# Optimization experiments

Hardware: AMD Instinct MI355X
Metric: run time of the kernel (lower is better)

The kernel has to match this reference:

```python
import jax, jax.numpy as jnp
import numpy as np

D_MODEL = 1024
NUM_HEADS = 16
HEAD_DIM = D_MODEL // NUM_HEADS
BATCH, SEQ = 2, 2048


def setup_inputs() -> dict:
    key = jax.random.key(0)
    ks = jax.random.split(key, 11)
    s = 1.0 / np.sqrt(D_MODEL)
    inp = {
        "query": jax.random.normal(ks[0], (BATCH, SEQ, D_MODEL), jnp.float32),
        "key": jax.random.normal(ks[1], (BATCH, SEQ, D_MODEL), jnp.float32),
        "value": jax.random.normal(ks[2], (BATCH, SEQ, D_MODEL), jnp.float32),
        "q_w": jax.random.uniform(ks[3], (D_MODEL, D_MODEL), jnp.float32, -s, s),
        "q_b": jax.random.uniform(ks[4], (D_MODEL,), jnp.float32, -s, s),
        "k_w": jax.random.uniform(ks[5], (D_MODEL, D_MODEL), jnp.float32, -s, s),
        "k_b": jax.random.uniform(ks[6], (D_MODEL,), jnp.float32, -s, s),
        "v_w": jax.random.uniform(ks[7], (D_MODEL, D_MODEL), jnp.float32, -s, s),
        "v_b": jax.random.uniform(ks[8], (D_MODEL,), jnp.float32, -s, s),
        "o_w": jax.random.uniform(ks[9], (D_MODEL, D_MODEL), jnp.float32, -s, s),
        "o_b": jax.random.uniform(ks[10], (D_MODEL,), jnp.float32, -s, s),
    }
    return inp


def reference(query, key, value, q_w, q_b, k_w, k_b, v_w, v_b, o_w, o_b):
    B = query.shape[0]
    # linear projections (torch Linear: x @ W^T + b)
    q = query @ q_w.T + q_b
    k = key @ k_w.T + k_b
    v = value @ v_w.T + v_b
    # split heads: [B, S, D] -> [B, H, S, Hd]
    def split(x):
        return x.reshape(B, -1, NUM_HEADS, HEAD_DIM).transpose(0, 2, 1, 3)
    q, k, v = split(q), split(k), split(v)
    scores = jnp.einsum("bhqd,bhkd->bhqk", q, k) / np.sqrt(HEAD_DIM).astype(np.float32)
    attn = jax.nn.softmax(scores, axis=-1)
    out = jnp.einsum("bhqk,bhkd->bhqd", attn, v)  # [B,H,S,Hd]
    merged = out.transpose(0, 2, 1, 3).reshape(B, -1, D_MODEL)
    return merged @ o_w.T + o_b
```

## Files before the change

kernel.cpp:

```cpp
#include <hip/hip_runtime.h>
#include <hip/hip_bf16.h>

typedef unsigned short u16;
typedef unsigned int u32;
typedef __attribute__((ext_vector_type(8))) short short8;
typedef __attribute__((ext_vector_type(4))) short s16x4;
typedef __attribute__((ext_vector_type(4))) float f32x4;
typedef __attribute__((ext_vector_type(4))) u32 u32v4;

__device__ __forceinline__ u16 f2bf(float f) {
    u32 u = __float_as_uint(f);
    return (u16)((u + 0x7FFFu + ((u >> 16) & 1u)) >> 16);
}
__device__ __forceinline__ u32 pack2bf(float a, float b) {
    __hip_bfloat162 h = __float22bfloat162_rn(float2{a, b});
    return *reinterpret_cast<u32*>(&h);
}
__device__ __forceinline__ float exp2hw(float x) {
    float r;
    asm("v_exp_f32 %0, %1" : "=v"(r) : "v"(x));
    return r;
}

__device__ __forceinline__ void gload16(const void* g, void* s) {
    __builtin_amdgcn_global_load_lds(
        (const __attribute__((address_space(1))) void*)g,
        (__attribute__((address_space(3))) void*)s, 16, 0, 0);
}

__global__ __launch_bounds__(256) void cast_all_kernel(
    const float* __restrict__ s0, const float* __restrict__ s1, const float* __restrict__ s2,
    const float* __restrict__ s3, const float* __restrict__ s4, const float* __restrict__ s5,
    const float* __restrict__ s6,
    u16* __restrict__ d0, u16* __restrict__ d1, u16* __restrict__ d2,
    u16* __restrict__ d3, u16* __restrict__ d4, u16* __restrict__ d5,
    u16* __restrict__ d6, int nBig, int nSmall)
{
    const int y = blockIdx.y;
    const float* s = y == 0 ? s0 : (y == 1 ? s1 : (y == 2 ? s2 : (y == 3 ? s3 : (y == 4 ? s4 : (y == 5 ? s5 : s6)))));
    u16* d = y == 0 ? d0 : (y == 1 ? d1 : (y == 2 ? d2 : (y == 3 ? d3 : (y == 4 ? d4 : (y == 5 ? d5 : d6)))));
    const int n = (y < 3) ? nBig : nSmall;
    int i = (blockIdx.x * 256 + threadIdx.x) * 4;
    const int stride = gridDim.x * 256 * 4;
    for (; i < n; i += stride) {
        float4 v = *(const float4*)(s + i);
        uint2 t;
        t.x = pack2bf(v.x, v.y);
        t.y = pack2bf(v.z, v.w);
        *(uint2*)(d + i) = t;
    }
}

__global__ __launch_bounds__(256) void qkv_gemm(
    const u16* __restrict__ Xq, const u16* __restrict__ Xk, const u16* __restrict__ Xv,
    const u16* __restrict__ Wqkv,
    const float* __restrict__ qb, const float* __restrict__ kb, const float* __restrict__ vb,
    u16* __restrict__ Qo, u16* __restrict__ Ko, u16* __restrict__ Vo)
{
    constexpr int K = 1024;
    __shared__ __align__(16) u16 Asm[2][4096];
    __shared__ __align__(16) u16 Bsm[2][4096];

    const int tid = threadIdx.x;
    const int wid = tid >> 6;
    const int lane = tid & 63;
    const int r15 = lane & 15, g = lane >> 4;
    const int flat = blockIdx.x;
    const int z = flat >> 8;
    const int fb = flat & 255;
    const int lsw = (fb & 7) * 32 + (fb >> 3);
    const int m0 = (lsw >> 3) * 128, n0 = (lsw & 7) * 128;
    const int nAll = (z << 10) + n0;
    const u16* A = z == 0 ? Xq : (z == 1 ? Xk : Xv);
    const int wr = wid >> 1, wc = wid & 1;

    f32x4 acc[4][4];
#pragma unroll
    for (int i = 0; i < 4; ++i)
#pragma unroll
        for (int j = 0; j < 4; ++j) acc[i][j] = (f32x4){0.f, 0.f, 0.f, 0.f};

    const int idx0 = tid, idx1 = tid + 256;
    const size_t aoff0 = (size_t)(m0 + (idx0 >> 2)) * K + (idx0 & 3) * 8;
    const size_t aoff1 = (size_t)(m0 + (idx1 >> 2)) * K + (idx1 & 3) * 8;
    const size_t boff0 = (size_t)(nAll + (idx0 >> 2)) * K + (idx0 & 3) * 8;
    const size_t boff1 = (size_t)(nAll + (idx1 >> 2)) * K + (idx1 & 3) * 8;
    const u16* abase = &Asm[0][0] + (wr * 64 + r15) * 32 + g * 8;
    const u16* bbase = &Bsm[0][0] + (wc * 64 + r15) * 32 + g * 8;

    gload16(A + aoff0, &Asm[0][wid * 512]);
    gload16(A + aoff1, &Asm[0][2048 + wid * 512]);
    gload16(Wqkv + boff0, &Bsm[0][wid * 512]);
    gload16(Wqkv + boff1, &Bsm[0][2048 + wid * 512]);
    __syncthreads();

#pragma unroll 2
    for (int t = 0; t < 32; ++t) {
        const int buf = t & 1;
        if (t < 31) {
            const int kt = (t + 1) * 32;
            gload16(A + aoff0 + kt, &Asm[buf ^ 1][wid * 512]);
            gload16(A + aoff1 + kt, &Asm[buf ^ 1][2048 + wid * 512]);
            gload16(Wqkv + boff0 + kt, &Bsm[buf ^ 1][wid * 512]);
            gload16(Wqkv + boff1 + kt, &Bsm[buf ^ 1][2048 + wid * 512]);
        }
        short8 af[4], bfr[4];
#pragma unroll
        for (int i = 0; i < 4; ++i) {
            af[i]  = *(const short8*)(abase + buf * 4096 + i * 512);
            bfr[i] = *(const short8*)(bbase + buf * 4096 + i * 512);
        }
#pragma unroll
        for (int i = 0; i < 4; ++i)
#pragma unroll
            for (int j = 0; j < 4; ++j)
                acc[i][j] = __builtin_amdgcn_mfma_f32_16x16x32_bf16(af[i], bfr[j], acc[i][j], 0, 0, 0);
        __syncthreads();
    }

    const float scale = (z == 0) ? 0.125f * 1.4426950408889634f : 1.0f;
    u16* ob = z == 0 ? Qo : (z == 1 ? Ko : Vo);
    const float* bias = z == 0 ? qb : (z == 1 ? kb : vb);
#pragma unroll
    for (int i = 0; i < 4; ++i) {
        const int mbase = m0 + wr * 64 + i * 16 + g * 4;
#pragma unroll
        for (int j = 0; j < 4; ++j) {
            const int n = n0 + wc * 64 + j * 16 + r15;
            const float bb = bias[n];
            if (z < 2) {
#pragma unroll
                for (int r = 0; r < 4; ++r)
                    ob[(size_t)(mbase + r) * 1024 + n] = f2bf((acc[i][j][r] + bb) * scale);
            } else {
                const int b_ = mbase >> 11, s_ = mbase & 2047;
                const int blk = (s_ >> 2) & 7;
                const int pb = ((blk & 3) << 1) | (blk >> 2);
                const int s_new = (s_ & ~31) | (pb << 2);
                s16x4 pk;
#pragma unroll
                for (int r = 0; r < 4; ++r) pk[r] = (short)f2bf(acc[i][j][r] + bb);
                *(s16x4*)(ob + ((size_t)b_ << 21) + (size_t)n * 2048 + s_new) = pk;
            }
        }
    }
}

__global__ __launch_bounds__(256) void o_gemm(
    const u16* __restrict__ A, const u16* __restrict__ W,
    const float* __restrict__ bias, float* __restrict__ outp)
{
    constexpr int N = 1024, K = 1024;
    __shared__ __align__(16) u16 Asm[2][4096];
    __shared__ __align__(16) u16 Bsm[2][4096];
    const int tid = threadIdx.x;
    const int wid = tid >> 6;
    const int lane = tid & 63;
    const int r15 = lane & 15, g = lane >> 4;
    const int fb = blockIdx.y * 8 + blockIdx.x;
    const int lsw = (fb & 7) * 32 + (fb >> 3);
    const int m0 = (lsw >> 3) * 128, n0 = (lsw & 7) * 128;
    const int wr = wid >> 1, wc = wid & 1;

    f32x4 acc[4][4];
#pragma unroll
    for (int i = 0; i < 4; ++i)
#pragma unroll
        for (int j = 0; j < 4; ++j) acc[i][j] = (f32x4){0.f, 0.f, 0.f, 0.f};

    const int idx0 = tid, idx1 = tid + 256;
    const size_t aoff0 = (size_t)(m0 + (idx0 >> 2)) * K + (idx0 & 3) * 8;
    const size_t aoff1 = (size_t)(m0 + (idx1 >> 2)) * K + (idx1 & 3) * 8;
    const size_t boff0 = (size_t)(n0 + (idx0 >> 2)) * K + (idx0 & 3) * 8;
    const size_t boff1 = (size_t)(n0 + (idx1 >> 2)) * K + (idx1 & 3) * 8;
    const u16* abase = &Asm[0][0] + (wr * 64 + r15) * 32 + g * 8;
    const u16* bbase = &Bsm[0][0] + (wc * 64 + r15) * 32 + g * 8;

    gload16(A + aoff0, &Asm[0][wid * 512]);
    gload16(A + aoff1, &Asm[0][2048 + wid * 512]);
    gload16(W + boff0, &Bsm[0][wid * 512]);
    gload16(W + boff1, &Bsm[0][2048 + wid * 512]);
    __syncthreads();

#pragma unroll 2
    for (int t = 0; t < 32; ++t) {
        const int buf = t & 1;
        if (t < 31) {
            const int kt = (t + 1) * 32;
            gload16(A + aoff0 + kt, &Asm[buf ^ 1][wid * 512]);
            gload16(A + aoff1 + kt, &Asm[buf ^ 1][2048 + wid * 512]);
            gload16(W + boff0 + kt, &Bsm[buf ^ 1][wid * 512]);
            gload16(W + boff1 + kt, &Bsm[buf ^ 1][2048 + wid * 512]);
        }
        short8 af[4], bfr[4];
#pragma unroll
        for (int i = 0; i < 4; ++i) {
            af[i]  = *(const short8*)(abase + buf * 4096 + i * 512);
            bfr[i] = *(const short8*)(bbase + buf * 4096 + i * 512);
        }
#pragma unroll
        for (int i = 0; i < 4; ++i)
#pragma unroll
            for (int j = 0; j < 4; ++j)
                acc[i][j] = __builtin_amdgcn_mfma_f32_16x16x32_bf16(af[i], bfr[j], acc[i][j], 0, 0, 0);
        __syncthreads();
    }

#pragma unroll
    for (int i = 0; i < 4; ++i) {
        const int mbase = m0 + wr * 64 + i * 16 + g * 4;
#pragma unroll
        for (int j = 0; j < 4; ++j) {
            const int n = n0 + wc * 64 + j * 16 + r15;
            const float bb = bias[n];
#pragma unroll
            for (int r = 0; r < 4; ++r)
                outp[(size_t)(mbase + r) * N + n] = acc[i][j][r] + bb;
        }
    }
}

__global__ __launch_bounds__(256) void attn_kernel(
    const u16* __restrict__ Q, const u16* __restrict__ Kb,
    const u16* __restrict__ Vt, u16* __restrict__ Mo)
{
    __shared__ __align__(16) u16 Ksm[2][4096];
    __shared__ __align__(16) u16 Vsm[2][4096];
    const int tid = threadIdx.x;
    const int wid = tid >> 6, lane = tid & 63;
    const int r15 = lane & 15, g = lane >> 4;
    const int bid = blockIdx.x;
    const int l = (bid & 7) * 64 + (bid >> 3);
    const int bh = l >> 4;
    const int b = bh >> 4, h = bh & 15;
    const int q0 = (l & 15) * 128 + wid * 32;

    const u16* Qbase = Q + ((size_t)b * 2048 + q0) * 1024 + h * 64;
    short8 qf[2][2];
#pragma unroll
    for (int qt = 0; qt < 2; ++qt)
#pragma unroll
        for (int f = 0; f < 2; ++f)
            qf[qt][f] = *(const short8*)(Qbase + (size_t)(qt * 16 + r15) * 1024 + f * 32 + g * 8);

    const int p0 = tid, p1 = tid + 256;
    const int row0 = p0 >> 3, slot0s = (p0 & 7) ^ (row0 & 7);
    const int row1 = p1 >> 3, slot1s = (p1 & 7) ^ (row1 & 7);
    const u16* Ks0 = Kb + ((size_t)b * 2048 + row0) * 1024 + h * 64 + slot0s * 8;
    const u16* Ks1 = Kb + ((size_t)b * 2048 + row1) * 1024 + h * 64 + slot1s * 8;
    const u16* Vs0 = Vt + ((size_t)b << 21) + (size_t)(h * 64 + row0) * 2048 + slot0s * 8;
    const u16* Vs1 = Vt + ((size_t)b << 21) + (size_t)(h * 64 + row1) * 2048 + slot1s * 8;

    const int sA = r15 & 7;
    const int sl0 = (g ^ sA) * 8;
    const int sl1 = sl0 ^ 32;
    const u16* kb0 = &Ksm[0][0] + r15 * 64 + sl0;
    const u16* kb1 = &Ksm[0][0] + r15 * 64 + sl1;
    const u16* vb0 = &Vsm[0][0] + r15 * 64 + sl0;
    const u16* vb1 = &Vsm[0][0] + r15 * 64 + sl1;

    f32x4 acc[2][4];
#pragma unroll
    for (int qt = 0; qt < 2; ++qt)
#pragma unroll
        for (int d4 = 0; d4 < 4; ++d4) acc[qt][d4] = (f32x4){0.f, 0.f, 0.f, 0.f};
    f32x4 accl[2] = {(f32x4){0.f, 0.f, 0.f, 0.f}, (f32x4){0.f, 0.f, 0.f, 0.f}};
    const short8 vone = {0x3F80, 0x3F80, 0x3F80, 0x3F80, 0x3F80, 0x3F80, 0x3F80, 0x3F80};

    gload16(Ks0, &Ksm[0][wid * 512]);
    gload16(Ks1, &Ksm[0][2048 + wid * 512]);
    gload16(Vs0, &Vsm[0][wid * 512]);
    gload16(Vs1, &Vsm[0][2048 + wid * 512]);
    Ks0 += 65536; Ks1 += 65536; Vs0 += 64; Vs1 += 64;
    __syncthreads();

#pragma unroll 2
    for (int t = 0; t < 32; ++t) {
        const int buf = t & 1;
        if (t < 31) {
            gload16(Ks0, &Ksm[buf ^ 1][wid * 512]);
            gload16(Ks1, &Ksm[buf ^ 1][2048 + wid * 512]);
            gload16(Vs0, &Vsm[buf ^ 1][wid * 512]);
            gload16(Vs1, &Vsm[buf ^ 1][2048 + wid * 512]);
            Ks0 += 65536; Ks1 += 65536; Vs0 += 64; Vs1 += 64;
        }

        short8 kf[4][2];
#pragma unroll
        for (int kt = 0; kt < 4; ++kt) {
            kf[kt][0] = *(const short8*)(kb0 + buf * 4096 + kt * 1024);
            kf[kt][1] = *(const short8*)(kb1 + buf * 4096 + kt * 1024);
        }

        f32x4 st[2][4];
#pragma unroll
        for (int qt = 0; qt < 2; ++qt)
#pragma unroll
            for (int kt = 0; kt < 4; ++kt) {
                f32x4 zz = (f32x4){0.f, 0.f, 0.f, 0.f};
                zz = __builtin_amdgcn_mfma_f32_16x16x32_bf16(kf[kt][0], qf[qt][0], zz, 0, 0, 0);
                zz = __builtin_amdgcn_mfma_f32_16x16x32_bf16(kf[kt][1], qf[qt][1], zz, 0, 0, 0);
                st[qt][kt] = zz;
            }

        u32v4 pA[2], pB[2];
#pragma unroll
        for (int qt = 0; qt < 2; ++qt) {
#pragma unroll
            for (int kt = 0; kt < 4; ++kt) {
                float e0 = exp2hw(st[qt][kt][0]);
                float e1 = exp2hw(st[qt][kt][1]);
                float e2 = exp2hw(st[qt][kt][2]);
                float e3 = exp2hw(st[qt][kt][3]);
                u32 lo = pack2bf(e0, e1);
                u32 hi = pack2bf(e2, e3);
                if (kt < 2) { pA[qt][kt * 2] = lo; pA[qt][kt * 2 + 1] = hi; }
                else        { pB[qt][(kt - 2) * 2] = lo; pB[qt][(kt - 2) * 2 + 1] = hi; }
            }
        }

        accl[0] = __builtin_amdgcn_mfma_f32_16x16x32_bf16(vone, __builtin_bit_cast(short8, pA[0]), accl[0], 0, 0, 0);
        accl[0] = __builtin_amdgcn_mfma_f32_16x16x32_bf16(vone, __builtin_bit_cast(short8, pB[0]), accl[0], 0, 0, 0);
        accl[1] = __builtin_amdgcn_mfma_f32_16x16x32_bf16(vone, __builtin_bit_cast(short8, pA[1]), accl[1], 0, 0, 0);
        accl[1] = __builtin_amdgcn_mfma_f32_16x16x32_bf16(vone, __builtin_bit_cast(short8, pB[1]), accl[1], 0, 0, 0);

#pragma unroll
        for (int d4 = 0; d4 < 4; ++d4) {
            short8 vf0 = *(const short8*)(vb0 + buf * 4096 + d4 * 1024);
            short8 vf1 = *(const short8*)(vb1 + buf * 4096 + d4 * 1024);
            acc[0][d4] = __builtin_amdgcn_mfma_f32_16x16x32_bf16(vf0, __builtin_bit_cast(short8, pA[0]), acc[0][d4], 0, 0, 0);
            acc[0][d4] = __builtin_amdgcn_mfma_f32_16x16x32_bf16(vf1, __builtin_bit_cast(short8, pB[0]), acc[0][d4], 0, 0, 0);
            acc[1][d4] = __builtin_amdgcn_mfma_f32_16x16x32_bf16(vf0, __builtin_bit_cast(short8, pA[1]), acc[1][d4], 0, 0, 0);
            acc[1][d4] = __builtin_amdgcn_mfma_f32_16x16x32_bf16(vf1, __builtin_bit_cast(short8, pB[1]), acc[1][d4], 0, 0, 0);
        }
        __syncthreads();
    }

#pragma unroll
    for (int qt = 0; qt < 2; ++qt) {
        const float inv = 1.f / accl[qt][0];
        const size_t orow = ((size_t)b * 2048 + q0 + qt * 16 + r15) * 1024 + h * 64;
#pragma unroll
        for (int d4 = 0; d4 < 4; ++d4) {
            uint2 o;
            o.x = pack2bf(acc[qt][d4][0] * inv, acc[qt][d4][1] * inv);
            o.y = pack2bf(acc[qt][d4][2] * inv, acc[qt][d4][3] * inv);
            *(uint2*)(Mo + orow + d4 * 16 + g * 4) = o;
        }
    }
}

extern "C" void kernel_launch(void* const* d_in, const int* in_sizes, int n_in,
                              void* d_out, int out_size, void* d_ws, size_t ws_size,
                              hipStream_t stream) {
    (void)in_sizes; (void)n_in; (void)out_size; (void)ws_size;
    const float* query = (const float*)d_in[0];
    const float* key   = (const float*)d_in[1];
    const float* value = (const float*)d_in[2];
    const float* q_w = (const float*)d_in[3];
    const float* q_b = (const float*)d_in[4];
    const float* k_w = (const float*)d_in[5];
    const float* k_b = (const float*)d_in[6];
    const float* v_w = (const float*)d_in[7];
    const float* v_b = (const float*)d_in[8];
    const float* o_w = (const float*)d_in[9];
    const float* o_b = (const float*)d_in[10];

    const size_t NE = (size_t)4096 * 1024;
    const size_t MW = (size_t)1024 * 1024;
    u16* w = (u16*)d_ws;
    u16* Xq = w;
    u16* Xk = Xq + NE;
    u16* Xv = Xk + NE;
    u16* Wq = Xv + NE;
    u16* Wk = Wq + MW;
    u16* Wv = Wk + MW;
    u16* Wo = Wv + MW;
    u16* Qb = Wo + MW;
    u16* Kb = Qb + NE;
    u16* Vt = Kb + NE;
    u16* Mo = Vt + NE;

    cast_all_kernel<<<dim3(2048, 7), 256, 0, stream>>>(
        query, key, value, q_w, k_w, v_w, o_w,
        Xq, Xk, Xv, Wq, Wk, Wv, Wo, (int)NE, (int)MW);
    qkv_gemm<<<dim3(768), 256, 0, stream>>>(
        Xq, Xk, Xv, Wq, q_b, k_b, v_b, Qb, Kb, Vt);
    attn_kernel<<<dim3(512), 256, 0, stream>>>(Qb, Kb, Vt, Mo);
    o_gemm<<<dim3(8, 32), 256, 0, stream>>>(Mo, Wo, o_b, (float*)d_out);
}
```

Before: 141.1 us.

## Use single-wave 64x64 GEMM blocks with swizzled LDS and waitcnt sync

```diff
diff --git a/kernel.cpp b/kernel.cpp
--- a/kernel.cpp
+++ b/kernel.cpp
@@ -27,6 +27,10 @@
         (const __attribute__((address_space(1))) void*)g,
         (__attribute__((address_space(3))) void*)s, 16, 0, 0);
 }
+
+#define VMW8() asm volatile("s_waitcnt vmcnt(8)" ::: "memory")
+#define VMW0() asm volatile("s_waitcnt vmcnt(0)" ::: "memory")
+#define LGK0() asm volatile("s_waitcnt lgkmcnt(0)" ::: "memory")
 
 __global__ __launch_bounds__(256) void cast_all_kernel(
     const float* __restrict__ s0, const float* __restrict__ s1, const float* __restrict__ s2,
@@ -51,28 +55,30 @@
     }
 }
 
-__global__ __launch_bounds__(256) void qkv_gemm(
+__global__ __launch_bounds__(64) void qkv_gemm(
     const u16* __restrict__ Xq, const u16* __restrict__ Xk, const u16* __restrict__ Xv,
     const u16* __restrict__ Wqkv,
     const float* __restrict__ qb, const float* __restrict__ kb, const float* __restrict__ vb,
     u16* __restrict__ Qo, u16* __restrict__ Ko, u16* __restrict__ Vo)
 {
-    constexpr int K = 1024;
-    __shared__ __align__(16) u16 Asm[2][4096];
-    __shared__ __align__(16) u16 Bsm[2][4096];
-
-    const int tid = threadIdx.x;
-    const int wid = tid >> 6;
-    const int lane = tid & 63;
+    __shared__ __align__(16) u16 Asm[2][2048];
+    __shared__ __align__(16) u16 Bsm[2][2048];
+    const int lane = threadIdx.x;
     const int r15 = lane & 15, g = lane >> 4;
-    const int flat = blockIdx.x;
-    const int z = flat >> 8;
-    const int fb = flat & 255;
-    const int lsw = (fb & 7) * 32 + (fb >> 3);
-    const int m0 = (lsw >> 3) * 128, n0 = (lsw & 7) * 128;
+    const int bid = blockIdx.x;
+    const int z = bid >> 10;
+    const int bl = bid & 1023;
+    const int mi = (bl & 7) * 8 + ((bl >> 3) & 7);
+    const int ni = bl >> 6;
+    const int m0 = mi * 64, n0 = ni * 64;
     const int nAll = (z << 10) + n0;
     const u16* A = z == 0 ? Xq : (z == 1 ? Xk : Xv);
-    const int wr = wid >> 1, wc = wid & 1;
+
+    const int srow = lane >> 2;
+    const int sslot = (lane & 3) ^ ((srow ^ (srow >> 2)) & 3);
+    const size_t aoff = (size_t)(m0 + srow) * 1024 + sslot * 8;
+    const size_t boff = (size_t)(nAll + srow) * 1024 + sslot * 8;
+    const int rsl = (g ^ ((r15 ^ (r15 >> 2)) & 3)) * 8;
 
     f32x4 acc[4][4];
 #pragma unroll
@@ -80,42 +86,32 @@
 #pragma unroll
         for (int j = 0; j < 4; ++j) acc[i][j] = (f32x4){0.f, 0.f, 0.f, 0.f};
 
-    const int idx0 = tid, idx1 = tid + 256;
-    const size_t aoff0 = (size_t)(m0 + (idx0 >> 2)) * K + (idx0 & 3) * 8;
-    const size_t aoff1 = (size_t)(m0 + (idx1 >> 2)) * K + (idx1 & 3) * 8;
-    const size_t boff0 = (size_t)(nAll + (idx0 >> 2)) * K + (idx0 & 3) * 8;
-    const size_t boff1 = (size_t)(nAll + (idx1 >> 2)) * K + (idx1 & 3) * 8;
-    const u16* abase = &Asm[0][0] + (wr * 64 + r15) * 32 + g * 8;
-    const u16* bbase = &Bsm[0][0] + (wc * 64 + r15) * 32 + g * 8;
-
-    gload16(A + aoff0, &Asm[0][wid * 512]);
-    gload16(A + aoff1, &Asm[0][2048 + wid * 512]);
-    gload16(Wqkv + boff0, &Bsm[0][wid * 512]);
-    gload16(Wqkv + boff1, &Bsm[0][2048 + wid * 512]);
-    __syncthreads();
-
+    auto STAGE = [&](int buf, int kt) {
+#pragma unroll
+        for (int j = 0; j < 4; ++j) {
+            gload16(A + aoff + j * 16384 + kt, &Asm[buf][j * 512]);
+            gload16(Wqkv + boff + j * 16384 + kt, &Bsm[buf][j * 512]);
+        }
+    };
+
+    STAGE(0, 0);
 #pragma unroll 2
     for (int t = 0; t < 32; ++t) {
         const int buf = t & 1;
-        if (t < 31) {
-            const int kt = (t + 1) * 32;
-            gload16(A + aoff0 + kt, &Asm[buf ^ 1][wid * 512]);
-            gload16(A + aoff1 + kt, &Asm[buf ^ 1][2048 + wid * 512]);
-            gload16(Wqkv + boff0 + kt, &Bsm[buf ^ 1][wid * 512]);
-            gload16(Wqkv + boff1 + kt, &Bsm[buf ^ 1][2048 + wid * 512]);
-        }
-        short8 af[4], bfr[4];
+        if (t < 31) { STAGE(buf ^ 1, (t + 1) * 32); VMW8(); }
+        else        { VMW0(); }
+        short8 af[4], bf[4];
 #pragma unroll
         for (int i = 0; i < 4; ++i) {
-            af[i]  = *(const short8*)(abase + buf * 4096 + i * 512);
-            bfr[i] = *(const short8*)(bbase + buf * 4096 + i * 512);
-        }
+            af[i] = *(const short8*)(&Asm[buf][i * 512 + r15 * 32 + rsl]);
+            bf[i] = *(const short8*)(&Bsm[buf][i * 512 + r15 * 32 + rsl]);
+        }
+        LGK0();
 #pragma unroll
         for (int i = 0; i < 4; ++i)
 #pragma unroll
             for (int j = 0; j < 4; ++j)
-                acc[i][j] = __builtin_amdgcn_mfma_f32_16x16x32_bf16(af[i], bfr[j], acc[i][j], 0, 0, 0);
-        __syncthreads();
+                acc[i][j] = __builtin_amdgcn_mfma_f32_16x16x32_bf16(af[i], bf[j], acc[i][j], 0, 0, 0);
     }
 
     const float scale = (z == 0) ? 0.125f * 1.4426950408889634f : 1.0f;
@@ -123,10 +119,10 @@
     const float* bias = z == 0 ? qb : (z == 1 ? kb : vb);
 #pragma unroll
     for (int i = 0; i < 4; ++i) {
-        const int mbase = m0 + wr * 64 + i * 16 + g * 4;
+        const int mbase = m0 + i * 16 + g * 4;
 #pragma unroll
         for (int j = 0; j < 4; ++j) {
-            const int n = n0 + wc * 64 + j * 16 + r15;
+            const int n = n0 + j * 16 + r15;
             const float bb = bias[n];
             if (z < 2) {
 #pragma unroll
@@ -146,21 +142,24 @@
     }
 }
 
-__global__ __launch_bounds__(256) void o_gemm(
+__global__ __launch_bounds__(64) void o_gemm(
     const u16* __restrict__ A, const u16* __restrict__ W,
     const float* __restrict__ bias, float* __restrict__ outp)
 {
-    constexpr int N = 1024, K = 1024;
-    __shared__ __align__(16) u16 Asm[2][4096];
-    __shared__ __align__(16) u16 Bsm[2][4096];
-    const int tid = threadIdx.x;
-    const int wid = tid >> 6;
-    const int lane = tid & 63;
+    __shared__ __align__(16) u16 Asm[2][2048];
+    __shared__ __align__(16) u16 Bsm[2][2048];
+    const int lane = threadIdx.x;
     const int r15 = lane & 15, g = lane >> 4;
-    const int fb = blockIdx.y * 8 + blockIdx.x;
-    const int lsw = (fb & 7) * 32 + (fb >> 3);
-    const int m0 = (lsw >> 3) * 128, n0 = (lsw & 7) * 128;
-    const int wr = wid >> 1, wc = wid & 1;
+    const int bl = blockIdx.x;
+    const int mi = (bl & 7) * 8 + ((bl >> 3) & 7);
+    const int ni = bl >> 6;
+    const int m0 = mi * 64, n0 = ni * 64;
+
+    const int srow = lane >> 2;
+    const int sslot = (lane & 3) ^ ((srow ^ (srow >> 2)) & 3);
+    const size_t aoff = (size_t)(m0 + srow) * 1024 + sslot * 8;
+    const size_t boff = (size_t)(n0 + srow) * 1024 + sslot * 8;
+    const int rsl = (g ^ ((r15 ^ (r15 >> 2)) & 3)) * 8;
 
     f32x4 acc[4][4];
 #pragma unroll
@@ -168,54 +167,44 @@
 #pragma unroll
         for (int j = 0; j < 4; ++j) acc[i][j] = (f32x4){0.f, 0.f, 0.f, 0.f};
 
-    const int idx0 = tid, idx1 = tid + 256;
-    const size_t aoff0 = (size_t)(m0 + (idx0 >> 2)) * K + (idx0 & 3) * 8;
-    const size_t aoff1 = (size_t)(m0 + (idx1 >> 2)) * K + (idx1 & 3) * 8;
-    const size_t boff0 = (size_t)(n0 + (idx0 >> 2)) * K + (idx0 & 3) * 8;
-    const size_t boff1 = (size_t)(n0 + (idx1 >> 2)) * K + (idx1 & 3) * 8;
-    const u16* abase = &Asm[0][0] + (wr * 64 + r15) * 32 + g * 8;
-    const u16* bbase = &Bsm[0][0] + (wc * 64 + r15) * 32 + g * 8;
-
-    gload16(A + aoff0, &Asm[0][wid * 512]);
-    gload16(A + aoff1, &Asm[0][2048 + wid * 512]);
-    gload16(W + boff0, &Bsm[0][wid * 512]);
-    gload16(W + boff1, &Bsm[0][2048 + wid * 512]);
-    __syncthreads();
-
+    auto STAGE = [&](int buf, int kt) {
+#pragma unroll
+        for (int j = 0; j < 4; ++j) {
+            gload16(A + aoff + j * 16384 + kt, &Asm[buf][j * 512]);
+            gload16(W + boff + j * 16384 + kt, &Bsm[buf][j * 512]);
+        }
+    };
+
+    STAGE(0, 0);
 #pragma unroll 2
     for (int t = 0; t < 32; ++t) {
         const int buf = t & 1;
-        if (t < 31) {
-            const int kt = (t + 1) * 32;
-            gload16(A + aoff0 + kt, &Asm[buf ^ 1][wid * 512]);
-            gload16(A + aoff1 + kt, &Asm[buf ^ 1][2048 + wid * 512]);
-            gload16(W + boff0 + kt, &Bsm[buf ^ 1][wid * 512]);
-            gload16(W + boff1 + kt, &Bsm[buf ^ 1][2048 + wid * 512]);
-        }
-        short8 af[4], bfr[4];
+        if (t < 31) { STAGE(buf ^ 1, (t + 1) * 32); VMW8(); }
+        else        { VMW0(); }
+        short8 af[4], bf[4];
 #pragma unroll
         for (int i = 0; i < 4; ++i) {
-            af[i]  = *(const short8*)(abase + buf * 4096 + i * 512);
-            bfr[i] = *(const short8*)(bbase + buf * 4096 + i * 512);
-        }
+            af[i] = *(const short8*)(&Asm[buf][i * 512 + r15 * 32 + rsl]);
+            bf[i] = *(const short8*)(&Bsm[buf][i * 512 + r15 * 32 + rsl]);
+        }
+        LGK0();
 #pragma unroll
         for (int i = 0; i < 4; ++i)
 #pragma unroll
             for (int j = 0; j < 4; ++j)
-                acc[i][j] = __builtin_amdgcn_mfma_f32_16x16x32_bf16(af[i], bfr[j], acc[i][j], 0, 0, 0);
-        __syncthreads();
+                acc[i][j] = __builtin_amdgcn_mfma_f32_16x16x32_bf16(af[i], bf[j], acc[i][j], 0, 0, 0);
     }
 
 #pragma unroll
     for (int i = 0; i < 4; ++i) {
-        const int mbase = m0 + wr * 64 + i * 16 + g * 4;
+        const int mbase = m0 + i * 16 + g * 4;
 #pragma unroll
         for (int j = 0; j < 4; ++j) {
-            const int n = n0 + wc * 64 + j * 16 + r15;
+            const int n = n0 + j * 16 + r15;
             const float bb = bias[n];
 #pragma unroll
             for (int r = 0; r < 4; ++r)
-                outp[(size_t)(mbase + r) * N + n] = acc[i][j][r] + bb;
+                outp[(size_t)(mbase + r) * 1024 + n] = acc[i][j][r] + bb;
         }
     }
 }
@@ -384,8 +373,8 @@
     cast_all_kernel<<<dim3(2048, 7), 256, 0, stream>>>(
         query, key, value, q_w, k_w, v_w, o_w,
         Xq, Xk, Xv, Wq, Wk, Wv, Wo, (int)NE, (int)MW);
-    qkv_gemm<<<dim3(768), 256, 0, stream>>>(
+    qkv_gemm<<<dim3(3072), 64, 0, stream>>>(
         Xq, Xk, Xv, Wq, q_b, k_b, v_b, Qb, Kb, Vt);
     attn_kernel<<<dim3(512), 256, 0, stream>>>(Qb, Kb, Vt, Mo);
-    o_gemm<<<dim3(8, 32), 256, 0, stream>>>(Mo, Wo, o_b, (float*)d_out);
-}
+    o_gemm<<<dim3(1024), 64, 0, stream>>>(Mo, Wo, o_b, (float*)d_out);
+}
```

After: 135.7 us. 1.04x faster.
